# Performance work log

Measured on AMD Instinct MI355X. Metric: run time of the kernel, lower is better.

## Reference

```python
import jax, jax.numpy as jnp
import numpy as np

H, W, D, HEADS = 32, 32, 16, 8
EPS = 1e-5

def _ln(x, g, b):
    m = jnp.mean(x, -1, keepdims=True)
    v = jnp.mean((x - m) ** 2, -1, keepdims=True)
    return (x - m) / jnp.sqrt(v + EPS) * g + b

def _attn(x, w_qkv, w_proj, b_proj):
    # x: (Bb, N, C); torch Linear: y = x @ W.T + b
    Bb, N, C = x.shape
    hd = C // HEADS
    qkv = jnp.einsum('bnc,dc->bnd', x, w_qkv).reshape(Bb, N, 3, HEADS, hd)
    q, k, v = qkv[:, :, 0], qkv[:, :, 1], qkv[:, :, 2]  # (Bb,N,h,hd)
    att = jnp.einsum('bnhd,bmhd->bhnm', q, k) * (hd ** -0.5)
    att = jax.nn.softmax(att, axis=-1)
    o = jnp.einsum('bhnm,bmhd->bnhd', att, v).reshape(Bb, N, C)
    return jnp.einsum('bnc,dc->bnd', o, w_proj) + b_proj

def setup_inputs() -> dict:
    key = jax.random.key(0)
    ks = jax.random.split(key, 8)
    C, HID = 96, 384
    s = 0.02
    return {
        'x': jax.random.normal(ks[0], (1, C, D, H, W), jnp.float32),
        'norm1_g': jnp.ones((C,), jnp.float32),
        'norm1_b': jnp.zeros((C,), jnp.float32),
        'qkv_hw_w': jax.random.normal(ks[1], (3 * C, C), jnp.float32) * s,
        'proj_hw_w': jax.random.normal(ks[2], (C, C), jnp.float32) * s,
        'proj_hw_b': jnp.zeros((C,), jnp.float32),
        'qkv_t_w': jax.random.normal(ks[3], (3 * C, C), jnp.float32) * s,
        'proj_t_w': jax.random.normal(ks[4], (C, C), jnp.float32) * s,
        'proj_t_b': jnp.zeros((C,), jnp.float32),
        'norm2_g': jnp.ones((C,), jnp.float32),
        'norm2_b': jnp.zeros((C,), jnp.float32),
        'fc1_w': jax.random.normal(ks[5], (HID, C), jnp.float32) * s,
        'fc1_b': jnp.zeros((HID,), jnp.float32),
        'fc2_w': jax.random.normal(ks[6], (C, HID), jnp.float32) * s,
        'fc2_b': jnp.zeros((C,), jnp.float32),
    }

def reference(x, norm1_g, norm1_b, qkv_hw_w, proj_hw_w, proj_hw_b,
              qkv_t_w, proj_t_w, proj_t_b, norm2_g, norm2_b,
              fc1_w, fc1_b, fc2_w, fc2_b):
    B, C = x.shape[0], x.shape[1]
    HWn = H * W
    xf = x.reshape(B, C, -1).transpose(0, 2, 1)  # (B, L, C), L = D*H*W (D-major)
    shortcut = xf
    n1 = _ln(xf, norm1_g, norm1_b).reshape(B, D, HWn, C)
    # attention over H*W tokens (batched over B*D)
    a_hw = _attn(n1.reshape(B * D, HWn, C), qkv_hw_w, proj_hw_w, proj_hw_b)
    a_hw = a_hw.reshape(B, -1, C)  # D-major token order
    # attention over D tokens (batched over B*H*W)
    a_t = _attn(n1.transpose(0, 2, 1, 3).reshape(B * HWn, D, C), qkv_t_w, proj_t_w, proj_t_b)
    a_t = a_t.reshape(B, HWn * D, C)  # HW-major order (faithful to original view)
    out_res = shortcut + a_hw + a_t
    h1 = jax.nn.gelu(jnp.einsum('blc,hc->blh', _ln(out_res, norm2_g, norm2_b), fc1_w) + fc1_b,
                     approximate=False)
    mlp_out = jnp.einsum('blh,ch->blc', h1, fc2_w) + fc2_b
    out_ffn = out_res + mlp_out
    out = out_ffn.reshape(B, H, W, D, C).transpose(0, 4, 3, 1, 2)  # (B,C,D,H,W)
    return out
```

## Files before the change

### kernel.cpp

```cpp
#include <hip/hip_runtime.h>
#include <math.h>

#define L_TOK 16384
#define C_DIM 96
#define N_HEADS 8
#define HD 12
#define D_DIM 16
#define HW_N 1024
#define HID_DIM 384
#define SCALE 0.2886751345948129f
#define LOG2E 1.4426950408889634f

typedef _Float16 h4 __attribute__((ext_vector_type(4)));
typedef __fp16 fp16x2 __attribute__((ext_vector_type(2)));
typedef float v4f __attribute__((ext_vector_type(4)));

static __device__ __forceinline__ float fast_exp2(float x) {
#if __has_builtin(__builtin_amdgcn_exp2f)
    return __builtin_amdgcn_exp2f(x);
#else
    float r;
    asm("v_exp_f32 %0, %1" : "=v"(r) : "v"(x));
    return r;
#endif
}

static __device__ __forceinline__ h4 pack4(float a, float b, float c, float d) {
    fp16x2 lo = __builtin_amdgcn_cvt_pkrtz(a, b);
    fp16x2 hi = __builtin_amdgcn_cvt_pkrtz(c, d);
    union { fp16x2 p[2]; h4 v; } u;
    u.p[0] = lo; u.p[1] = hi;
    return u.v;
}

__global__ __launch_bounds__(256) void prep_kernel(
    const float* __restrict__ x, const float* __restrict__ g1,
    const float* __restrict__ b1, _Float16* __restrict__ n1h,
    const float* __restrict__ qkv_hw_w, const float* __restrict__ qkv_t_w,
    const float* __restrict__ proj_hw_w, const float* __restrict__ proj_t_w,
    const float* __restrict__ proj_hw_b, const float* __restrict__ proj_t_b,
    const float* __restrict__ fc1_w, const float* __restrict__ fc2_w,
    _Float16* __restrict__ wq, _Float16* __restrict__ wp,
    _Float16* __restrict__ wf1, _Float16* __restrict__ wf2,
    float* __restrict__ bp) {
    if (blockIdx.x < 64) {
        int l = blockIdx.x * 256 + threadIdx.x;
        float v[C_DIM];
        float s = 0.f;
#pragma unroll
        for (int c = 0; c < C_DIM; c++) {
            v[c] = x[(size_t)c * L_TOK + l];
            s += v[c];
        }
        float mean = s * (1.f / C_DIM);
        float var = 0.f;
#pragma unroll
        for (int c = 0; c < C_DIM; c++) {
            float dd = v[c] - mean;
            var += dd * dd;
        }
        float r = rsqrtf(var * (1.f / C_DIM) + 1e-5f);
        _Float16* op = n1h + (size_t)l * C_DIM;
#pragma unroll
        for (int c = 0; c < C_DIM; c += 4) {
            h4 o;
            o[0] = (_Float16)((v[c + 0] - mean) * r * g1[c + 0] + b1[c + 0]);
            o[1] = (_Float16)((v[c + 1] - mean) * r * g1[c + 1] + b1[c + 1]);
            o[2] = (_Float16)((v[c + 2] - mean) * r * g1[c + 2] + b1[c + 2]);
            o[3] = (_Float16)((v[c + 3] - mean) * r * g1[c + 3] + b1[c + 3]);
            *(h4*)(op + c) = o;
        }
        return;
    }
    int idx = (blockIdx.x - 64) * 256 + threadIdx.x;
    if (idx < 55296) {
        int n = idx / 96;
        float v = (n < 288) ? qkv_hw_w[idx] : qkv_t_w[idx - 27648];
        bool isq = (n < 96) || (n >= 288 && n < 384);
        wq[idx] = (_Float16)(isq ? v * (SCALE * LOG2E) : v);
    } else if (idx < 55296 + 18432) {
        int i = idx - 55296;
        int n = i / 192, k = i % 192;
        float v = (k < 96) ? proj_hw_w[n * 96 + k] : proj_t_w[n * 96 + k - 96];
        wp[i] = (_Float16)v;
    } else if (idx < 73728 + 36864) {
        int i = idx - 73728;
        wf1[i] = (_Float16)fc1_w[i];
    } else if (idx < 110592 + 36864) {
        int i = idx - 110592;
        wf2[i] = (_Float16)fc2_w[i];
    } else if (idx < 147456 + 96) {
        int i = idx - 147456;
        bp[i] = proj_hw_b[i] + proj_t_b[i];
    }
}

#define GBM 64
#define GBN 48
#define GBK 96
#define LSTRIDE 104

__global__ __launch_bounds__(256) void gemm_qkv(
    const _Float16* __restrict__ A, const _Float16* __restrict__ W,
    _Float16* __restrict__ Qp, _Float16* __restrict__ Kp,
    _Float16* __restrict__ VTp, _Float16* __restrict__ Tp) {
    __shared__ _Float16 As[GBM][LSTRIDE];
    __shared__ _Float16 Ws[GBN][LSTRIDE];
    const int t = threadIdx.x;
    const int m0 = blockIdx.x * GBM;
    const int n0 = blockIdx.y * GBN;
    const int lane = t & 63, w = t >> 6, g = lane >> 4, r = lane & 15;

    v4f acc[3];
#pragma unroll
    for (int nt = 0; nt < 3; nt++) {
        acc[nt][0] = 0.f; acc[nt][1] = 0.f; acc[nt][2] = 0.f; acc[nt][3] = 0.f;
    }
#pragma unroll
    for (int i = 0; i < 3; i++) {
        int idx = t + i * 256;
        int row = idx / 12, c = idx % 12;
        *(float4*)&As[row][c * 8] =
            *(const float4*)&A[(size_t)(m0 + row) * 96 + c * 8];
    }
#pragma unroll
    for (int i = 0; i < 3; i++) {
        int idx = t + i * 256;
        if (idx < 576) {
            int row = idx / 12, c = idx % 12;
            *(float4*)&Ws[row][c * 8] =
                *(const float4*)&W[(size_t)(n0 + row) * 96 + c * 8];
        }
    }
    __syncthreads();
#pragma unroll
    for (int ks = 0; ks < 6; ks++) {
        h4 af = *(const h4*)&As[w * 16 + r][ks * 16 + 4 * g];
#pragma unroll
        for (int nt = 0; nt < 3; nt++) {
            h4 wf = *(const h4*)&Ws[nt * 16 + r][ks * 16 + 4 * g];
            acc[nt] = __builtin_amdgcn_mfma_f32_16x16x16f16(wf, af, acc[nt], 0, 0, 0);
        }
    }

    const int m = m0 + w * 16 + r;
    const int d = m >> 10, hw = m & 1023;
    const int by = blockIdx.y;
#pragma unroll
    for (int nt = 0; nt < 3; nt++) {
        const int nb = n0 + nt * 16 + 4 * g;
        h4 ov;
        ov[0] = (_Float16)acc[nt][0]; ov[1] = (_Float16)acc[nt][1];
        ov[2] = (_Float16)acc[nt][2]; ov[3] = (_Float16)acc[nt][3];
        if (by < 2) {
            int n = nb;
            int h = (unsigned)n / 12u, dd = n - h * 12;
            *(h4*)&Qp[((size_t)(d * 8 + h) * 1024 + hw) * 12 + dd] = ov;
        } else if (by < 4) {
            int n = nb - 96;
            int h = (unsigned)n / 12u, dd = n - h * 12;
            *(h4*)&Kp[((size_t)(d * 8 + h) * 1024 + hw) * 12 + dd] = ov;
        } else if (by < 6) {
            int n = nb - 192;
            int h = (unsigned)n / 12u, dd = n - h * 12;
#pragma unroll
            for (int j = 0; j < 4; j++) {
                VTp[((size_t)(d * 8 + h) * 12 + dd + j) * 1024 + hw] = ov[j];
            }
        } else {
            *(h4*)&Tp[(size_t)(hw * 16 + d) * 288 + (nb - 288)] = ov;
        }
    }
}

__global__ __launch_bounds__(256) void gemm_proj_ln2(
    const _Float16* __restrict__ A, const _Float16* __restrict__ W,
    const float* __restrict__ bp, const float* __restrict__ x,
    const float* __restrict__ g2, const float* __restrict__ b2,
    float* __restrict__ out_res, _Float16* __restrict__ n2h) {
    __shared__ _Float16 As[64][LSTRIDE];
    __shared__ _Float16 Ws[96][LSTRIDE];
    const int t = threadIdx.x;
    const int m0 = blockIdx.x * 64;
    const int lane = t & 63, w = t >> 6, g = lane >> 4, r = lane & 15;

    v4f acc[6];
#pragma unroll
    for (int nt = 0; nt < 6; nt++) {
        acc[nt][0] = 0.f; acc[nt][1] = 0.f; acc[nt][2] = 0.f; acc[nt][3] = 0.f;
    }

    for (int k0 = 0; k0 < 192; k0 += 96) {
        __syncthreads();
#pragma unroll
        for (int i = 0; i < 3; i++) {
            int idx = t + i * 256;
            int row = idx / 12, c = idx % 12;
            *(float4*)&As[row][c * 8] =
                *(const float4*)&A[(size_t)(m0 + row) * 192 + k0 + c * 8];
        }
#pragma unroll
        for (int i = 0; i < 5; i++) {
            int idx = t + i * 256;
            if (idx < 1152) {
                int row = idx / 12, c = idx % 12;
                *(float4*)&Ws[row][c * 8] =
                    *(const float4*)&W[(size_t)row * 192 + k0 + c * 8];
            }
        }
        __syncthreads();
#pragma unroll
        for (int ks = 0; ks < 6; ks++) {
            h4 af = *(const h4*)&As[w * 16 + r][ks * 16 + 4 * g];
#pragma unroll
            for (int nt = 0; nt < 6; nt++) {
                h4 wf = *(const h4*)&Ws[nt * 16 + r][ks * 16 + 4 * g];
                acc[nt] =
                    __builtin_amdgcn_mfma_f32_16x16x16f16(wf, af, acc[nt], 0, 0, 0);
            }
        }
    }

    const int m = m0 + w * 16 + r;
    float v[24];
    float sum = 0.f;
#pragma unroll
    for (int nt = 0; nt < 6; nt++) {
        const int nb = nt * 16 + 4 * g;
        float4 bv = *(const float4*)&bp[nb];
        float a0 = acc[nt][0] + bv.x + x[(size_t)(nb + 0) * L_TOK + m];
        float a1 = acc[nt][1] + bv.y + x[(size_t)(nb + 1) * L_TOK + m];
        float a2 = acc[nt][2] + bv.z + x[(size_t)(nb + 2) * L_TOK + m];
        float a3 = acc[nt][3] + bv.w + x[(size_t)(nb + 3) * L_TOK + m];
        v[nt * 4 + 0] = a0; v[nt * 4 + 1] = a1;
        v[nt * 4 + 2] = a2; v[nt * 4 + 3] = a3;
        sum += (a0 + a1) + (a2 + a3);
        float4 ov; ov.x = a0; ov.y = a1; ov.z = a2; ov.w = a3;
        *(float4*)&out_res[(size_t)m * 96 + nb] = ov;
    }
    sum += __shfl_xor(sum, 16, 64);
    sum += __shfl_xor(sum, 32, 64);
    float mean = sum * (1.f / 96.f);
    float ss = 0.f;
#pragma unroll
    for (int i = 0; i < 24; i++) {
        float dd = v[i] - mean;
        ss += dd * dd;
    }
    ss += __shfl_xor(ss, 16, 64);
    ss += __shfl_xor(ss, 32, 64);
    float rstd = rsqrtf(ss * (1.f / 96.f) + 1e-5f);
#pragma unroll
    for (int nt = 0; nt < 6; nt++) {
        const int nb = nt * 16 + 4 * g;
        float4 gg = *(const float4*)&g2[nb];
        float4 bb = *(const float4*)&b2[nb];
        h4 o;
        o[0] = (_Float16)((v[nt * 4 + 0] - mean) * rstd * gg.x + bb.x);
        o[1] = (_Float16)((v[nt * 4 + 1] - mean) * rstd * gg.y + bb.y);
        o[2] = (_Float16)((v[nt * 4 + 2] - mean) * rstd * gg.z + bb.z);
        o[3] = (_Float16)((v[nt * 4 + 3] - mean) * rstd * gg.w + bb.w);
        *(h4*)&n2h[(size_t)m * 96 + nb] = o;
    }
}

__global__ __launch_bounds__(256) void gemm_fc1(
    const _Float16* __restrict__ A, const _Float16* __restrict__ W,
    const float* __restrict__ bias, _Float16* __restrict__ h1) {
    __shared__ _Float16 As[GBM][LSTRIDE];
    __shared__ _Float16 Ws[GBN][LSTRIDE];
    const int t = threadIdx.x;
    const int m0 = blockIdx.x * GBM;
    const int n0 = blockIdx.y * GBN;
    const int lane = t & 63, w = t >> 6, g = lane >> 4, r = lane & 15;

    v4f acc[3];
#pragma unroll
    for (int nt = 0; nt < 3; nt++) {
        acc[nt][0] = 0.f; acc[nt][1] = 0.f; acc[nt][2] = 0.f; acc[nt][3] = 0.f;
    }
#pragma unroll
    for (int i = 0; i < 3; i++) {
        int idx = t + i * 256;
        int row = idx / 12, c = idx % 12;
        *(float4*)&As[row][c * 8] =
            *(const float4*)&A[(size_t)(m0 + row) * 96 + c * 8];
    }
#pragma unroll
    for (int i = 0; i < 3; i++) {
        int idx = t + i * 256;
        if (idx < 576) {
            int row = idx / 12, c = idx % 12;
            *(float4*)&Ws[row][c * 8] =
                *(const float4*)&W[(size_t)(n0 + row) * 96 + c * 8];
        }
    }
    __syncthreads();
#pragma unroll
    for (int ks = 0; ks < 6; ks++) {
        h4 af = *(const h4*)&As[w * 16 + r][ks * 16 + 4 * g];
#pragma unroll
        for (int nt = 0; nt < 3; nt++) {
            h4 wf = *(const h4*)&Ws[nt * 16 + r][ks * 16 + 4 * g];
            acc[nt] = __builtin_amdgcn_mfma_f32_16x16x16f16(wf, af, acc[nt], 0, 0, 0);
        }
    }

    const int m = m0 + w * 16 + r;
#pragma unroll
    for (int nt = 0; nt < 3; nt++) {
        const int nb = n0 + nt * 16 + 4 * g;
        float4 bv = *(const float4*)&bias[nb];
        float vv[4];
        vv[0] = acc[nt][0] + bv.x; vv[1] = acc[nt][1] + bv.y;
        vv[2] = acc[nt][2] + bv.z; vv[3] = acc[nt][3] + bv.w;
        h4 ov;
#pragma unroll
        for (int j = 0; j < 4; j++) {
            float u = vv[j];
            ov[j] = (_Float16)(0.5f * u * (1.f + erff(u * 0.7071067811865476f)));
        }
        *(h4*)&h1[(size_t)m * 384 + nb] = ov;
    }
}

__global__ __launch_bounds__(256) void gemm_fc2(
    const _Float16* __restrict__ A, const _Float16* __restrict__ W,
    const float* __restrict__ bias, float* __restrict__ out,
    const float* __restrict__ res) {
    __shared__ _Float16 As[GBM][LSTRIDE];
    __shared__ _Float16 Ws[GBN][LSTRIDE];
    __shared__ float sh[GBN][68];
    const int t = threadIdx.x;
    const int bx = blockIdx.x;
    const int bxs = (bx & 7) * 32 + (bx >> 3);
    const int m0 = bxs * GBM;
    const int n0 = blockIdx.y * GBN;
    const int lane = t & 63, w = t >> 6, g = lane >> 4, r = lane & 15;

    v4f acc[3];
#pragma unroll
    for (int nt = 0; nt < 3; nt++) {
        acc[nt][0] = 0.f; acc[nt][1] = 0.f; acc[nt][2] = 0.f; acc[nt][3] = 0.f;
    }

    for (int k0 = 0; k0 < 384; k0 += GBK) {
        __syncthreads();
#pragma unroll
        for (int i = 0; i < 3; i++) {
            int idx = t + i * 256;
            int row = idx / 12, c = idx % 12;
            *(float4*)&As[row][c * 8] =
                *(const float4*)&A[(size_t)(m0 + row) * 384 + k0 + c * 8];
        }
#pragma unroll
        for (int i = 0; i < 3; i++) {
            int idx = t + i * 256;
            if (idx < 576) {
                int row = idx / 12, c = idx % 12;
                *(float4*)&Ws[row][c * 8] =
                    *(const float4*)&W[(size_t)(n0 + row) * 384 + k0 + c * 8];
            }
        }
        __syncthreads();
#pragma unroll
        for (int ks = 0; ks < 6; ks++) {
            h4 af = *(const h4*)&As[w * 16 + r][ks * 16 + 4 * g];
#pragma unroll
            for (int nt = 0; nt < 3; nt++) {
                h4 wf = *(const h4*)&Ws[nt * 16 + r][ks * 16 + 4 * g];
                acc[nt] =
                    __builtin_amdgcn_mfma_f32_16x16x16f16(wf, af, acc[nt], 0, 0, 0);
            }
        }
    }

    const int m = m0 + w * 16 + r;
    const int m_local = w * 16 + r;
#pragma unroll
    for (int nt = 0; nt < 3; nt++) {
        const int nb = n0 + nt * 16 + 4 * g;
        float4 bv = *(const float4*)&bias[nb];
        float4 rv = *(const float4*)&res[(size_t)m * 96 + nb];
        sh[nt * 16 + 4 * g + 0][m_local] = acc[nt][0] + bv.x + rv.x;
        sh[nt * 16 + 4 * g + 1][m_local] = acc[nt][1] + bv.y + rv.y;
        sh[nt * 16 + 4 * g + 2][m_local] = acc[nt][2] + bv.z + rv.z;
        sh[nt * 16 + 4 * g + 3][m_local] = acc[nt][3] + bv.w + rv.w;
    }
    __syncthreads();
    const int hh = m0 >> 9, ww0 = (m0 >> 4) & 31;
#pragma unroll
    for (int i = 0; i < 3; i++) {
        int task = t + i * 256;
        int n_local = task >> 4, dd = task & 15;
        float4 ov;
        ov.x = sh[n_local][dd];
        ov.y = sh[n_local][dd + 16];
        ov.z = sh[n_local][dd + 32];
        ov.w = sh[n_local][dd + 48];
        *(float4*)&out[(size_t)(n0 + n_local) * L_TOK + dd * 1024 + hh * 32 + ww0] = ov;
    }
}

__global__ __launch_bounds__(256) void attn_hw_kernel(
    const _Float16* __restrict__ Qp, const _Float16* __restrict__ Kp,
    const _Float16* __restrict__ VTp, _Float16* __restrict__ o_cat) {
    __shared__ _Float16 K_lds[1024 * 12];
    __shared__ _Float16 VT_lds[13 * 1032];
    const int t = threadIdx.x;
    const int qb = blockIdx.x, h = blockIdx.y, d = blockIdx.z;
    const size_t tokbase = (size_t)d * HW_N;
    const int hoff = h * HD;
    const size_t slice = (size_t)(d * 8 + h);

    {
        const float4* Kg = (const float4*)(Kp + slice * 12288);
        float4* K4 = (float4*)K_lds;
#pragma unroll
        for (int i = 0; i < 6; i++) K4[t + i * 256] = Kg[t + i * 256];
        const float4* Vg = (const float4*)(VTp + slice * 12288);
#pragma unroll
        for (int i = 0; i < 6; i++) {
            int off = t + i * 256;
            int row = off >> 7, col = (off & 127) * 8;
            *(float4*)&VT_lds[row * 1032 + col] = Vg[off];
        }
        unsigned* zp = (unsigned*)&VT_lds[12 * 1032];
        zp[t] = 0x3C003C00u; zp[t + 256] = 0x3C003C00u;
        if (t < 4) zp[t + 512] = 0x3C003C00u;
    }

    const int lane = t & 63, w = t >> 6, g = lane >> 4, r = lane & 15;
    const int q0w = qb * 128 + w * 32;

    h4 zf; zf[0] = zf[1] = zf[2] = zf[3] = (_Float16)0.f;
    h4 qf[2];
    {
        const _Float16* Qbase = Qp + (slice * 1024 + q0w + r) * 12 + 4 * g;
#pragma unroll
        for (int qt = 0; qt < 2; qt++) {
            qf[qt] = (g < 3) ? *(const h4*)(Qbase + qt * 16 * 12) : zf;
        }
    }

    v4f acc[2];
#pragma unroll
    for (int qt = 0; qt < 2; qt++) {
        acc[qt][0] = acc[qt][1] = acc[qt][2] = acc[qt][3] = 0.f;
    }

    const int koff = r * 12 + 4 * g;
    const int rowc = (r < 12) ? r : 12;
    const int voff = rowc * 1032 + 4 * g;

    __syncthreads();

    v4f zero; zero[0] = zero[1] = zero[2] = zero[3] = 0.f;
#pragma unroll 4
    for (int kt = 0; kt < HW_N / 16; kt++) {
        h4 kf = (g < 3) ? *(const h4*)&K_lds[kt * 192 + koff] : zf;
        h4 vf = *(const h4*)&VT_lds[voff + kt * 16];
#pragma unroll
        for (int qt = 0; qt < 2; qt++) {
            v4f s = __builtin_amdgcn_mfma_f32_16x16x16f16(kf, qf[qt], zero, 0, 0, 0);
            h4 pf = pack4(fast_exp2(s[0]), fast_exp2(s[1]),
                          fast_exp2(s[2]), fast_exp2(s[3]));
            acc[qt] = __builtin_amdgcn_mfma_f32_16x16x16f16(vf, pf, acc[qt], 0, 0, 0);
        }
    }

#pragma unroll
    for (int qt = 0; qt < 2; qt++) {
        float denom = __shfl(acc[qt][0], 48 + r, 64);
        float rs = 1.f / denom;
        if (g < 3) {
            _Float16* op =
                o_cat + (tokbase + q0w + qt * 16 + r) * 192 + hoff + 4 * g;
            h4 o;
            o[0] = (_Float16)(acc[qt][0] * rs);
            o[1] = (_Float16)(acc[qt][1] * rs);
            o[2] = (_Float16)(acc[qt][2] * rs);
            o[3] = (_Float16)(acc[qt][3] * rs);
            *(h4*)op = o;
        }
    }
}

__global__ __launch_bounds__(256) void attn_t_kernel(
    const _Float16* __restrict__ Tp, _Float16* __restrict__ o_cat) {
    int gid = blockIdx.x * 256 + threadIdx.x;
    int hw = gid >> 7;
    int h = (gid >> 4) & 7;
    int q = gid & 15;
    const int hoff = h * HD;
    const _Float16* base = Tp + (size_t)(hw * 16) * 288;

    float qr[HD];
    {
        const _Float16* p = base + q * 288 + hoff;
        h4 a = *(const h4*)p, b = *(const h4*)(p + 4), c = *(const h4*)(p + 8);
#pragma unroll
        for (int e = 0; e < 4; e++) {
            qr[e] = (float)a[e]; qr[4 + e] = (float)b[e]; qr[8 + e] = (float)c[e];
        }
    }
    float s[D_DIM];
    float mx = -1e30f;
#pragma unroll
    for (int j = 0; j < D_DIM; j++) {
        const _Float16* kp = base + j * 288 + 96 + hoff;
        h4 a = *(const h4*)kp, b = *(const h4*)(kp + 4), c = *(const h4*)(kp + 8);
        float dot = 0.f;
#pragma unroll
        for (int e = 0; e < 4; e++) {
            dot += qr[e] * (float)a[e] + qr[4 + e] * (float)b[e] +
                   qr[8 + e] * (float)c[e];
        }
        s[j] = dot;
        mx = fmaxf(mx, dot);
    }
    float sum = 0.f;
#pragma unroll
    for (int j = 0; j < D_DIM; j++) {
        s[j] = fast_exp2(s[j] - mx);
        sum += s[j];
    }
    float rs = 1.f / sum;
    float o[HD];
#pragma unroll
    for (int e = 0; e < HD; e++) o[e] = 0.f;
#pragma unroll
    for (int j = 0; j < D_DIM; j++) {
        const _Float16* vp = base + j * 288 + 192 + hoff;
        h4 a = *(const h4*)vp, b = *(const h4*)(vp + 4), c = *(const h4*)(vp + 8);
        float p = s[j];
#pragma unroll
        for (int e = 0; e < 4; e++) {
            o[e] += p * (float)a[e];
            o[4 + e] += p * (float)b[e];
            o[8 + e] += p * (float)c[e];
        }
    }
    _Float16* op = o_cat + ((size_t)hw * D_DIM + q) * 192 + 96 + hoff;
#pragma unroll
    for (int e = 0; e < HD; e += 4) {
        h4 a;
        a[0] = (_Float16)(o[e] * rs); a[1] = (_Float16)(o[e + 1] * rs);
        a[2] = (_Float16)(o[e + 2] * rs); a[3] = (_Float16)(o[e + 3] * rs);
        *(h4*)(op + e) = a;
    }
}

extern "C" void kernel_launch(void* const* d_in, const int* in_sizes, int n_in,
                              void* d_out, int out_size, void* d_ws,
                              size_t ws_size, hipStream_t stream) {
    const float* x         = (const float*)d_in[0];
    const float* norm1_g   = (const float*)d_in[1];
    const float* norm1_b   = (const float*)d_in[2];
    const float* qkv_hw_w  = (const float*)d_in[3];
    const float* proj_hw_w = (const float*)d_in[4];
    const float* proj_hw_b = (const float*)d_in[5];
    const float* qkv_t_w   = (const float*)d_in[6];
    const float* proj_t_w  = (const float*)d_in[7];
    const float* proj_t_b  = (const float*)d_in[8];
    const float* norm2_g   = (const float*)d_in[9];
    const float* norm2_b   = (const float*)d_in[10];
    const float* fc1_w     = (const float*)d_in[11];
    const float* fc1_b     = (const float*)d_in[12];
    const float* fc2_w     = (const float*)d_in[13];
    const float* fc2_b     = (const float*)d_in[14];
    float* out = (float*)d_out;

    char* ws = (char*)d_ws;
    _Float16* n1h    = (_Float16*)ws;
    _Float16* o_cat  = n1h + (size_t)L_TOK * C_DIM;
    float*    out_res= (float*)(o_cat + (size_t)L_TOK * 192);
    _Float16* packs  = (_Float16*)(out_res + (size_t)L_TOK * C_DIM);
    _Float16* Qp     = packs;
    _Float16* Kp     = Qp + 1572864;
    _Float16* VTp    = Kp + 1572864;
    _Float16* Tp     = VTp + 1572864;
    _Float16* h1     = packs;
    _Float16* wq     = Tp + (size_t)L_TOK * 288;
    _Float16* wp     = wq + 55296;
    _Float16* wf1    = wp + 18432;
    _Float16* wf2    = wf1 + 36864;
    float*    bp     = (float*)(wf2 + 36864);

    prep_kernel<<<641, 256, 0, stream>>>(x, norm1_g, norm1_b, n1h,
                                         qkv_hw_w, qkv_t_w, proj_hw_w,
                                         proj_t_w, proj_hw_b, proj_t_b,
                                         fc1_w, fc2_w, wq, wp, wf1, wf2, bp);
    gemm_qkv<<<dim3(L_TOK / GBM, 576 / GBN), 256, 0, stream>>>(
        n1h, wq, Qp, Kp, VTp, Tp);
    attn_hw_kernel<<<dim3(8, N_HEADS, D_DIM), 256, 0, stream>>>(
        Qp, Kp, VTp, o_cat);
    attn_t_kernel<<<(HW_N * N_HEADS * D_DIM) / 256, 256, 0, stream>>>(Tp, o_cat);
    gemm_proj_ln2<<<L_TOK / 64, 256, 0, stream>>>(
        o_cat, wp, bp, x, norm2_g, norm2_b, out_res, n1h);
    gemm_fc1<<<dim3(L_TOK / GBM, HID_DIM / GBN), 256, 0, stream>>>(
        n1h, wf1, fc1_b, h1);
    gemm_fc2<<<dim3(L_TOK / GBM, C_DIM / GBN), 256, 0, stream>>>(
        h1, wf2, fc2_b, out, out_res);
}
```

Measured before the change: 94.20 us.

## Fuse projection, LN2, FC1+GELU and FC2 into a single per-tile kernel

Replaces three kernels (proj+LN2, fc1, fc2) with one kernel that keeps the 64-token tile's residual, LN2 output and GELU hidden activations on chip (hidden in registers, LN2 output in shared memory). This removes the global round-trips for out_res, n2h and the 16384x384 fp16 hidden tensor, plus two launches. The cost is that each block reloads all of fc1/fc2 weights from global memory, there are only 256 blocks, and register pressure is high (96 hidden fragments per thread plus accumulators), which may limit occupancy.

```diff
diff --git a/kernel.cpp b/kernel.cpp
--- a/kernel.cpp
+++ b/kernel.cpp
@@ -173,55 +173,62 @@
     }
 }
 
-__global__ __launch_bounds__(256) void gemm_proj_ln2(
-    const _Float16* __restrict__ A, const _Float16* __restrict__ W,
+__global__ __launch_bounds__(256) void fused_mlp(
+    const _Float16* __restrict__ A, const _Float16* __restrict__ wp,
     const float* __restrict__ bp, const float* __restrict__ x,
     const float* __restrict__ g2, const float* __restrict__ b2,
-    float* __restrict__ out_res, _Float16* __restrict__ n2h) {
-    __shared__ _Float16 As[64][LSTRIDE];
-    __shared__ _Float16 Ws[96][LSTRIDE];
+    const _Float16* __restrict__ wf1, const float* __restrict__ f1b,
+    const _Float16* __restrict__ wf2, const float* __restrict__ f2b,
+    float* __restrict__ out) {
+    __shared__ __align__(16) char pool[46592];
+    _Float16* Abuf = (_Float16*)pool;
+    _Float16* Wbuf = (_Float16*)(pool + 13312);
+    _Float16* N2   = (_Float16*)(pool + 33280);
+    float*    sh   = (float*)pool;
+
     const int t = threadIdx.x;
-    const int m0 = blockIdx.x * 64;
+    const int bx = blockIdx.x;
+    const int bxs = (bx & 7) * 32 + (bx >> 3);
+    const int m0 = bxs * 64;
     const int lane = t & 63, w = t >> 6, g = lane >> 4, r = lane & 15;
+    const int ml = w * 16 + r;
+    const int m = m0 + ml;
 
     v4f acc[6];
 #pragma unroll
     for (int nt = 0; nt < 6; nt++) {
         acc[nt][0] = 0.f; acc[nt][1] = 0.f; acc[nt][2] = 0.f; acc[nt][3] = 0.f;
     }
-
-    for (int k0 = 0; k0 < 192; k0 += 96) {
+    for (int kc = 0; kc < 2; kc++) {
         __syncthreads();
 #pragma unroll
         for (int i = 0; i < 3; i++) {
             int idx = t + i * 256;
             int row = idx / 12, c = idx % 12;
-            *(float4*)&As[row][c * 8] =
-                *(const float4*)&A[(size_t)(m0 + row) * 192 + k0 + c * 8];
+            *(float4*)&Abuf[row * LSTRIDE + c * 8] =
+                *(const float4*)&A[(size_t)(m0 + row) * 192 + kc * 96 + c * 8];
         }
 #pragma unroll
         for (int i = 0; i < 5; i++) {
             int idx = t + i * 256;
             if (idx < 1152) {
                 int row = idx / 12, c = idx % 12;
-                *(float4*)&Ws[row][c * 8] =
-                    *(const float4*)&W[(size_t)row * 192 + k0 + c * 8];
+                *(float4*)&Wbuf[row * LSTRIDE + c * 8] =
+                    *(const float4*)&wp[(size_t)row * 192 + kc * 96 + c * 8];
             }
         }
         __syncthreads();
 #pragma unroll
         for (int ks = 0; ks < 6; ks++) {
-            h4 af = *(const h4*)&As[w * 16 + r][ks * 16 + 4 * g];
+            h4 af = *(const h4*)&Abuf[ml * LSTRIDE + ks * 16 + 4 * g];
 #pragma unroll
             for (int nt = 0; nt < 6; nt++) {
-                h4 wf = *(const h4*)&Ws[nt * 16 + r][ks * 16 + 4 * g];
+                h4 wf = *(const h4*)&Wbuf[(nt * 16 + r) * LSTRIDE + ks * 16 + 4 * g];
                 acc[nt] =
                     __builtin_amdgcn_mfma_f32_16x16x16f16(wf, af, acc[nt], 0, 0, 0);
             }
         }
     }
-
-    const int m = m0 + w * 16 + r;
     float v[24];
     float sum = 0.f;
 #pragma unroll
@@ -235,8 +242,6 @@
         v[nt * 4 + 0] = a0; v[nt * 4 + 1] = a1;
         v[nt * 4 + 2] = a2; v[nt * 4 + 3] = a3;
         sum += (a0 + a1) + (a2 + a3);
-        float4 ov; ov.x = a0; ov.y = a1; ov.z = a2; ov.w = a3;
-        *(float4*)&out_res[(size_t)m * 96 + nb] = ov;
     }
     sum += __shfl_xor(sum, 16, 64);
     sum += __shfl_xor(sum, 32, 64);
@@ -260,145 +265,101 @@
         o[1] = (_Float16)((v[nt * 4 + 1] - mean) * rstd * gg.y + bb.y);
         o[2] = (_Float16)((v[nt * 4 + 2] - mean) * rstd * gg.z + bb.z);
         o[3] = (_Float16)((v[nt * 4 + 3] - mean) * rstd * gg.w + bb.w);
-        *(h4*)&n2h[(size_t)m * 96 + nb] = o;
-    }
-}
-
-__global__ __launch_bounds__(256) void gemm_fc1(
-    const _Float16* __restrict__ A, const _Float16* __restrict__ W,
-    const float* __restrict__ bias, _Float16* __restrict__ h1) {
-    __shared__ _Float16 As[GBM][LSTRIDE];
-    __shared__ _Float16 Ws[GBN][LSTRIDE];
-    const int t = threadIdx.x;
-    const int m0 = blockIdx.x * GBM;
-    const int n0 = blockIdx.y * GBN;
-    const int lane = t & 63, w = t >> 6, g = lane >> 4, r = lane & 15;
-
-    v4f acc[3];
-#pragma unroll
-    for (int nt = 0; nt < 3; nt++) {
-        acc[nt][0] = 0.f; acc[nt][1] = 0.f; acc[nt][2] = 0.f; acc[nt][3] = 0.f;
-    }
-#pragma unroll
-    for (int i = 0; i < 3; i++) {
-        int idx = t + i * 256;
-        int row = idx / 12, c = idx % 12;
-        *(float4*)&As[row][c * 8] =
-            *(const float4*)&A[(size_t)(m0 + row) * 96 + c * 8];
-    }
-#pragma unroll
-    for (int i = 0; i < 3; i++) {
-        int idx = t + i * 256;
-        if (idx < 576) {
-            int row = idx / 12, c = idx % 12;
-            *(float4*)&Ws[row][c * 8] =
-                *(const float4*)&W[(size_t)(n0 + row) * 96 + c * 8];
-        }
-    }
+        *(h4*)&N2[ml * LSTRIDE + nb] = o;
+    }
+
+    h4 hf[4][6];
+    for (int nc = 0; nc < 4; nc++) {
+        __syncthreads();
+#pragma unroll
+        for (int i = 0; i < 5; i++) {
+            int idx = t + i * 256;
+            if (idx < 1152) {
+                int row = idx / 12, c = idx % 12;
+                *(float4*)&Wbuf[row * LSTRIDE + c * 8] =
+                    *(const float4*)&wf1[(size_t)(nc * 96 + row) * 96 + c * 8];
+            }
+        }
+        __syncthreads();
+        v4f f[6];
+#pragma unroll
+        for (int nt = 0; nt < 6; nt++) {
+            f[nt][0] = 0.f; f[nt][1] = 0.f; f[nt][2] = 0.f; f[nt][3] = 0.f;
+        }
+#pragma unroll
+        for (int ks = 0; ks < 6; ks++) {
+            h4 af = *(const h4*)&N2[ml * LSTRIDE + ks * 16 + 4 * g];
+#pragma unroll
+            for (int nt = 0; nt < 6; nt++) {
+                h4 wf = *(const h4*)&Wbuf[(nt * 16 + r) * LSTRIDE + ks * 16 + 4 * g];
+                f[nt] = __builtin_amdgcn_mfma_f32_16x16x16f16(wf, af, f[nt], 0, 0, 0);
+            }
+        }
+#pragma unroll
+        for (int nt = 0; nt < 6; nt++) {
+            const int nb = nc * 96 + nt * 16 + 4 * g;
+            float4 bv = *(const float4*)&f1b[nb];
+            float u0 = f[nt][0] + bv.x, u1 = f[nt][1] + bv.y;
+            float u2 = f[nt][2] + bv.z, u3 = f[nt][3] + bv.w;
+            h4 o;
+            o[0] = (_Float16)(0.5f * u0 * (1.f + erff(u0 * 0.7071067811865476f)));
+            o[1] = (_Float16)(0.5f * u1 * (1.f + erff(u1 * 0.7071067811865476f)));
+            o[2] = (_Float16)(0.5f * u2 * (1.f + erff(u2 * 0.7071067811865476f)));
+            o[3] = (_Float16)(0.5f * u3 * (1.f + erff(u3 * 0.7071067811865476f)));
+            hf[nc][nt] = o;
+        }
+    }
+
+    v4f o6[6];
+#pragma unroll
+    for (int nt = 0; nt < 6; nt++) {
+        o6[nt][0] = 0.f; o6[nt][1] = 0.f; o6[nt][2] = 0.f; o6[nt][3] = 0.f;
+    }
+    for (int kc = 0; kc < 4; kc++) {
+        __syncthreads();
+#pragma unroll
+        for (int i = 0; i < 5; i++) {
+            int idx = t + i * 256;
+            if (idx < 1152) {
+                int row = idx / 12, c = idx % 12;
+                *(float4*)&Wbuf[row * LSTRIDE + c * 8] =
+                    *(const float4*)&wf2[(size_t)row * 384 + kc * 96 + c * 8];
+            }
+        }
+        __syncthreads();
+#pragma unroll
+        for (int ks = 0; ks < 6; ks++) {
+            h4 af = hf[kc][ks];
+#pragma unroll
+            for (int nt = 0; nt < 6; nt++) {
+                h4 wf = *(const h4*)&Wbuf[(nt * 16 + r) * LSTRIDE + ks * 16 + 4 * g];
+                o6[nt] = __builtin_amdgcn_mfma_f32_16x16x16f16(wf, af, o6[nt], 0, 0, 0);
+            }
+        }
+    }
+
     __syncthreads();
 #pragma unroll
-    for (int ks = 0; ks < 6; ks++) {
-        h4 af = *(const h4*)&As[w * 16 + r][ks * 16 + 4 * g];
-#pragma unroll
-        for (int nt = 0; nt < 3; nt++) {
-            h4 wf = *(const h4*)&Ws[nt * 16 + r][ks * 16 + 4 * g];
-            acc[nt] = __builtin_amdgcn_mfma_f32_16x16x16f16(wf, af, acc[nt], 0, 0, 0);
-        }
-    }
-
-    const int m = m0 + w * 16 + r;
-#pragma unroll
-    for (int nt = 0; nt < 3; nt++) {
-        const int nb = n0 + nt * 16 + 4 * g;
-        float4 bv = *(const float4*)&bias[nb];
-        float vv[4];
-        vv[0] = acc[nt][0] + bv.x; vv[1] = acc[nt][1] + bv.y;
-        vv[2] = acc[nt][2] + bv.z; vv[3] = acc[nt][3] + bv.w;
-        h4 ov;
-#pragma unroll
-        for (int j = 0; j < 4; j++) {
-            float u = vv[j];
-            ov[j] = (_Float16)(0.5f * u * (1.f + erff(u * 0.7071067811865476f)));
-        }
-        *(h4*)&h1[(size_t)m * 384 + nb] = ov;
-    }
-}
-
-__global__ __launch_bounds__(256) void gemm_fc2(
-    const _Float16* __restrict__ A, const _Float16* __restrict__ W,
-    const float* __restrict__ bias, float* __restrict__ out,
-    const float* __restrict__ res) {
-    __shared__ _Float16 As[GBM][LSTRIDE];
-    __shared__ _Float16 Ws[GBN][LSTRIDE];
-    __shared__ float sh[GBN][68];
-    const int t = threadIdx.x;
-    const int bx = blockIdx.x;
-    const int bxs = (bx & 7) * 32 + (bx >> 3);
-    const int m0 = bxs * GBM;
-    const int n0 = blockIdx.y * GBN;
-    const int lane = t & 63, w = t >> 6, g = lane >> 4, r = lane & 15;
-
-    v4f acc[3];
-#pragma unroll
-    for (int nt = 0; nt < 3; nt++) {
-        acc[nt][0] = 0.f; acc[nt][1] = 0.f; acc[nt][2] = 0.f; acc[nt][3] = 0.f;
-    }
-
-    for (int k0 = 0; k0 < 384; k0 += GBK) {
-        __syncthreads();
-#pragma unroll
-        for (int i = 0; i < 3; i++) {
-            int idx = t + i * 256;
-            int row = idx / 12, c = idx % 12;
-            *(float4*)&As[row][c * 8] =
-                *(const float4*)&A[(size_t)(m0 + row) * 384 + k0 + c * 8];
-        }
-#pragma unroll
-        for (int i = 0; i < 3; i++) {
-            int idx = t + i * 256;
-            if (idx < 576) {
-                int row = idx / 12, c = idx % 12;
-                *(float4*)&Ws[row][c * 8] =
-                    *(const float4*)&W[(size_t)(n0 + row) * 384 + k0 + c * 8];
-            }
-        }
-        __syncthreads();
-#pragma unroll
-        for (int ks = 0; ks < 6; ks++) {
-            h4 af = *(const h4*)&As[w * 16 + r][ks * 16 + 4 * g];
-#pragma unroll
-            for (int nt = 0; nt < 3; nt++) {
-                h4 wf = *(const h4*)&Ws[nt * 16 + r][ks * 16 + 4 * g];
-                acc[nt] =
-                    __builtin_amdgcn_mfma_f32_16x16x16f16(wf, af, acc[nt], 0, 0, 0);
-            }
-        }
-    }
-
-    const int m = m0 + w * 16 + r;
-    const int m_local = w * 16 + r;
-#pragma unroll
-    for (int nt = 0; nt < 3; nt++) {
-        const int nb = n0 + nt * 16 + 4 * g;
-        float4 bv = *(const float4*)&bias[nb];
-        float4 rv = *(const float4*)&res[(size_t)m * 96 + nb];
-        sh[nt * 16 + 4 * g + 0][m_local] = acc[nt][0] + bv.x + rv.x;
-        sh[nt * 16 + 4 * g + 1][m_local] = acc[nt][1] + bv.y + rv.y;
-        sh[nt * 16 + 4 * g + 2][m_local] = acc[nt][2] + bv.z + rv.z;
-        sh[nt * 16 + 4 * g + 3][m_local] = acc[nt][3] + bv.w + rv.w;
+    for (int nt = 0; nt < 6; nt++) {
+        const int nb = nt * 16 + 4 * g;
+        float4 bv = *(const float4*)&f2b[nb];
+        sh[(nb + 0) * 68 + ml] = o6[nt][0] + bv.x + v[nt * 4 + 0];
+        sh[(nb + 1) * 68 + ml] = o6[nt][1] + bv.y + v[nt * 4 + 1];
+        sh[(nb + 2) * 68 + ml] = o6[nt][2] + bv.z + v[nt * 4 + 2];
+        sh[(nb + 3) * 68 + ml] = o6[nt][3] + bv.w + v[nt * 4 + 3];
     }
     __syncthreads();
     const int hh = m0 >> 9, ww0 = (m0 >> 4) & 31;
 #pragma unroll
-    for (int i = 0; i < 3; i++) {
+    for (int i = 0; i < 6; i++) {
         int task = t + i * 256;
-        int n_local = task >> 4, dd = task & 15;
+        int n = task >> 4, dd = task & 15;
         float4 ov;
-        ov.x = sh[n_local][dd];
-        ov.y = sh[n_local][dd + 16];
-        ov.z = sh[n_local][dd + 32];
-        ov.w = sh[n_local][dd + 48];
-        *(float4*)&out[(size_t)(n0 + n_local) * L_TOK + dd * 1024 + hh * 32 + ww0] = ov;
+        ov.x = sh[n * 68 + dd];
+        ov.y = sh[n * 68 + dd + 16];
+        ov.z = sh[n * 68 + dd + 32];
+        ov.w = sh[n * 68 + dd + 48];
+        *(float4*)&out[(size_t)n * L_TOK + dd * 1024 + hh * 32 + ww0] = ov;
     }
 }
 
@@ -580,7 +541,6 @@
     _Float16* Kp     = Qp + 1572864;
     _Float16* VTp    = Kp + 1572864;
     _Float16* Tp     = VTp + 1572864;
-    _Float16* h1     = packs;
     _Float16* wq     = Tp + (size_t)L_TOK * 288;
     _Float16* wp     = wq + 55296;
     _Float16* wf1    = wp + 18432;
@@ -596,10 +556,6 @@
     attn_hw_kernel<<<dim3(8, N_HEADS, D_DIM), 256, 0, stream>>>(
         Qp, Kp, VTp, o_cat);
     attn_t_kernel<<<(HW_N * N_HEADS * D_DIM) / 256, 256, 0, stream>>>(Tp, o_cat);
-    gemm_proj_ln2<<<L_TOK / 64, 256, 0, stream>>>(
-        o_cat, wp, bp, x, norm2_g, norm2_b, out_res, n1h);
-    gemm_fc1<<<dim3(L_TOK / GBM, HID_DIM / GBN), 256, 0, stream>>>(
-        n1h, wf1, fc1_b, h1);
-    gemm_fc2<<<dim3(L_TOK / GBM, C_DIM / GBN), 256, 0, stream>>>(
-        h1, wf2, fc2_b, out, out_res);
-}
+    fused_mlp<<<L_TOK / 64, 256, 0, stream>>>(
+        o_cat, wp, bp, x, norm2_g, norm2_b, wf1, fc1_b, wf2, fc2_b, out);
+}
```

New measurement: 93.99 us. About the same (-0.2%).

## Split proj+LN2 GEMM across column halves with 32-row tiles and double-buffered weights

Applied to the files above, without the earlier changes.

The fused projection + LayerNorm2 kernel now processes 32 rows per block instead of 64, and splits the 96 output columns between pairs of waves. Row statistics are combined across the two waves through shared memory. The whole A tile is loaded once and both K-halves of the weight get their own buffers, which removes a sync round. The variance now comes from a single pass (sum and sum of squares). This doubles the grid for better occupancy and latency hiding, at the cost of reloading the full weight matrix per block and slightly less numerically robust variance.

```diff
diff --git a/kernel.cpp b/kernel.cpp
--- a/kernel.cpp
+++ b/kernel.cpp
@@ -174,93 +174,112 @@
 }
 
 __global__ __launch_bounds__(256) void gemm_proj_ln2(
-    const _Float16* __restrict__ A, const _Float16* __restrict__ W,
+    const _Float16* __restrict__ A, const _Float16* __restrict__ wpw,
     const float* __restrict__ bp, const float* __restrict__ x,
     const float* __restrict__ g2, const float* __restrict__ b2,
     float* __restrict__ out_res, _Float16* __restrict__ n2h) {
-    __shared__ _Float16 As[64][LSTRIDE];
-    __shared__ _Float16 Ws[96][LSTRIDE];
+    __shared__ _Float16 As[32 * 200];
+    __shared__ _Float16 Ws[2][96 * LSTRIDE];
+    __shared__ float red[2][32][2];
+
     const int t = threadIdx.x;
-    const int m0 = blockIdx.x * 64;
+    const int m0 = blockIdx.x * 32;
     const int lane = t & 63, w = t >> 6, g = lane >> 4, r = lane & 15;
-
-    v4f acc[6];
-#pragma unroll
-    for (int nt = 0; nt < 6; nt++) {
+    const int mrow = (w >> 1) * 16, ch = w & 1;
+    const int rl = mrow + r;
+    const int m = m0 + rl;
+
+#pragma unroll
+    for (int i = 0; i < 3; i++) {
+        int idx = t + i * 256;
+        int row = idx / 24, c = idx % 24;
+        *(float4*)&As[row * 200 + c * 8] =
+            *(const float4*)&A[(size_t)(m0 + row) * 192 + c * 8];
+    }
+#pragma unroll
+    for (int i = 0; i < 5; i++) {
+        int idx = t + i * 256;
+        if (idx < 1152) {
+            int row = idx / 12, c = idx % 12;
+            *(float4*)&Ws[0][row * LSTRIDE + c * 8] =
+                *(const float4*)&wpw[(size_t)row * 192 + c * 8];
+        }
+    }
+    __syncthreads();
+#pragma unroll
+    for (int i = 0; i < 5; i++) {
+        int idx = t + i * 256;
+        if (idx < 1152) {
+            int row = idx / 12, c = idx % 12;
+            *(float4*)&Ws[1][row * LSTRIDE + c * 8] =
+                *(const float4*)&wpw[(size_t)row * 192 + 96 + c * 8];
+        }
+    }
+    v4f acc[3];
+#pragma unroll
+    for (int nt = 0; nt < 3; nt++) {
         acc[nt][0] = 0.f; acc[nt][1] = 0.f; acc[nt][2] = 0.f; acc[nt][3] = 0.f;
     }
-
-    for (int k0 = 0; k0 < 192; k0 += 96) {
-        __syncthreads();
-#pragma unroll
-        for (int i = 0; i < 3; i++) {
-            int idx = t + i * 256;
-            int row = idx / 12, c = idx % 12;
-            *(float4*)&As[row][c * 8] =
-                *(const float4*)&A[(size_t)(m0 + row) * 192 + k0 + c * 8];
-        }
-#pragma unroll
-        for (int i = 0; i < 5; i++) {
-            int idx = t + i * 256;
-            if (idx < 1152) {
-                int row = idx / 12, c = idx % 12;
-                *(float4*)&Ws[row][c * 8] =
-                    *(const float4*)&W[(size_t)row * 192 + k0 + c * 8];
-            }
-        }
-        __syncthreads();
-#pragma unroll
-        for (int ks = 0; ks < 6; ks++) {
-            h4 af = *(const h4*)&As[w * 16 + r][ks * 16 + 4 * g];
-#pragma unroll
-            for (int nt = 0; nt < 6; nt++) {
-                h4 wf = *(const h4*)&Ws[nt * 16 + r][ks * 16 + 4 * g];
-                acc[nt] =
-                    __builtin_amdgcn_mfma_f32_16x16x16f16(wf, af, acc[nt], 0, 0, 0);
-            }
-        }
-    }
-
-    const int m = m0 + w * 16 + r;
-    float v[24];
-    float sum = 0.f;
-#pragma unroll
-    for (int nt = 0; nt < 6; nt++) {
-        const int nb = nt * 16 + 4 * g;
-        float4 bv = *(const float4*)&bp[nb];
-        float a0 = acc[nt][0] + bv.x + x[(size_t)(nb + 0) * L_TOK + m];
-        float a1 = acc[nt][1] + bv.y + x[(size_t)(nb + 1) * L_TOK + m];
-        float a2 = acc[nt][2] + bv.z + x[(size_t)(nb + 2) * L_TOK + m];
-        float a3 = acc[nt][3] + bv.w + x[(size_t)(nb + 3) * L_TOK + m];
+#pragma unroll
+    for (int ks = 0; ks < 6; ks++) {
+        h4 af = *(const h4*)&As[rl * 200 + ks * 16 + 4 * g];
+#pragma unroll
+        for (int nt = 0; nt < 3; nt++) {
+            h4 wf = *(const h4*)&Ws[0][(ch * 48 + nt * 16 + r) * LSTRIDE +
+                                       ks * 16 + 4 * g];
+            acc[nt] = __builtin_amdgcn_mfma_f32_16x16x16f16(wf, af, acc[nt], 0, 0, 0);
+        }
+    }
+    __syncthreads();
+#pragma unroll
+    for (int ks = 0; ks < 6; ks++) {
+        h4 af = *(const h4*)&As[rl * 200 + 96 + ks * 16 + 4 * g];
+#pragma unroll
+        for (int nt = 0; nt < 3; nt++) {
+            h4 wf = *(const h4*)&Ws[1][(ch * 48 + nt * 16 + r) * LSTRIDE +
+                                       ks * 16 + 4 * g];
+            acc[nt] = __builtin_amdgcn_mfma_f32_16x16x16f16(wf, af, acc[nt], 0, 0, 0);
+        }
+    }
+
+    float v[12];
+    float s1 = 0.f, s2 = 0.f;
+#pragma unroll
+    for (int nt = 0; nt < 3; nt++) {
+        const int c = ch * 48 + nt * 16 + 4 * g;
+        float4 bv = *(const float4*)&bp[c];
+        float a0 = acc[nt][0] + bv.x + x[(size_t)(c + 0) * L_TOK + m];
+        float a1 = acc[nt][1] + bv.y + x[(size_t)(c + 1) * L_TOK + m];
+        float a2 = acc[nt][2] + bv.z + x[(size_t)(c + 2) * L_TOK + m];
+        float a3 = acc[nt][3] + bv.w + x[(size_t)(c + 3) * L_TOK + m];
         v[nt * 4 + 0] = a0; v[nt * 4 + 1] = a1;
         v[nt * 4 + 2] = a2; v[nt * 4 + 3] = a3;
-        sum += (a0 + a1) + (a2 + a3);
+        s1 += (a0 + a1) + (a2 + a3);
+        s2 += (a0 * a0 + a1 * a1) + (a2 * a2 + a3 * a3);
         float4 ov; ov.x = a0; ov.y = a1; ov.z = a2; ov.w = a3;
-        *(float4*)&out_res[(size_t)m * 96 + nb] = ov;
-    }
-    sum += __shfl_xor(sum, 16, 64);
-    sum += __shfl_xor(sum, 32, 64);
-    float mean = sum * (1.f / 96.f);
-    float ss = 0.f;
-#pragma unroll
-    for (int i = 0; i < 24; i++) {
-        float dd = v[i] - mean;
-        ss += dd * dd;
-    }
-    ss += __shfl_xor(ss, 16, 64);
-    ss += __shfl_xor(ss, 32, 64);
-    float rstd = rsqrtf(ss * (1.f / 96.f) + 1e-5f);
-#pragma unroll
-    for (int nt = 0; nt < 6; nt++) {
-        const int nb = nt * 16 + 4 * g;
-        float4 gg = *(const float4*)&g2[nb];
-        float4 bb = *(const float4*)&b2[nb];
-        h4 o;
-        o[0] = (_Float16)((v[nt * 4 + 0] - mean) * rstd * gg.x + bb.x);
-        o[1] = (_Float16)((v[nt * 4 + 1] - mean) * rstd * gg.y + bb.y);
-        o[2] = (_Float16)((v[nt * 4 + 2] - mean) * rstd * gg.z + bb.z);
-        o[3] = (_Float16)((v[nt * 4 + 3] - mean) * rstd * gg.w + bb.w);
-        *(h4*)&n2h[(size_t)m * 96 + nb] = o;
+        *(float4*)&out_res[(size_t)m * 96 + c] = ov;
+    }
+    s1 += __shfl_xor(s1, 16, 64);
+    s1 += __shfl_xor(s1, 32, 64);
+    s2 += __shfl_xor(s2, 16, 64);
+    s2 += __shfl_xor(s2, 32, 64);
+    if (g == 0) { red[ch][rl][0] = s1; red[ch][rl][1] = s2; }
+    __syncthreads();
+    float t1 = red[0][rl][0] + red[1][rl][0];
+    float t2 = red[0][rl][1] + red[1][rl][1];
+    float mean = t1 * (1.f / 96.f);
+    float var = t2 * (1.f / 96.f) - mean * mean;
+    float rstd = rsqrtf(var + 1e-5f);
+#pragma unroll
+    for (int nt = 0; nt < 3; nt++) {
+        const int c = ch * 48 + nt * 16 + 4 * g;
+        float4 gg = *(const float4*)&g2[c];
+        float4 bb = *(const float4*)&b2[c];
+        h4 o = pack4((v[nt * 4 + 0] - mean) * rstd * gg.x + bb.x,
+                     (v[nt * 4 + 1] - mean) * rstd * gg.y + bb.y,
+                     (v[nt * 4 + 2] - mean) * rstd * gg.z + bb.z,
+                     (v[nt * 4 + 3] - mean) * rstd * gg.w + bb.w);
+        *(h4*)&n2h[(size_t)m * 96 + c] = o;
     }
 }
 
@@ -596,7 +615,7 @@
     attn_hw_kernel<<<dim3(8, N_HEADS, D_DIM), 256, 0, stream>>>(
         Qp, Kp, VTp, o_cat);
     attn_t_kernel<<<(HW_N * N_HEADS * D_DIM) / 256, 256, 0, stream>>>(Tp, o_cat);
-    gemm_proj_ln2<<<L_TOK / 64, 256, 0, stream>>>(
+    gemm_proj_ln2<<<L_TOK / 32, 256, 0, stream>>>(
         o_cat, wp, bp, x, norm2_g, norm2_b, out_res, n1h);
     gemm_fc1<<<dim3(L_TOK / GBM, HID_DIM / GBN), 256, 0, stream>>>(
         n1h, wf1, fc1_b, h1);
```

Result: no change. 93.15 us (-1.1%).
